# Performance work log

Hardware: AMD Instinct MI355X
Metric: run time of the kernel (lower is better)

Reference implementation:

```python
import jax, jax.numpy as jnp
import numpy as np

N = 100000      # nodes
E = 1600000     # edges (avg degree 16)
NX = 3          # input feature dim (data.x.shape[1])
K = 2           # number of kernels (len(kernel_DD) = manifold dim)
ORDER = 2       # par['order']
DEPTH = 2       # par['depth']
EPS = 1e-12     # F.normalize eps


def setup_inputs() -> dict:
    key = jax.random.key(0)
    ks = jax.random.split(key, 10)
    x = jax.random.normal(ks[0], (N, NX), dtype=jnp.float32)
    # per-edge kernel weights for the k directional kernels (sparse N x N ops)
    K_DD_vals = 0.1 * jax.random.normal(ks[1], (K, E), dtype=jnp.float32)
    K_DA_vals = 0.1 * jax.random.normal(ks[2], (K, E), dtype=jnp.float32)
    # lin[0]: in = 18*k = 36, out = 72
    lin0_w = 0.05 * jax.random.normal(ks[3], (36, 72), dtype=jnp.float32)
    lin0_b = jnp.zeros((72,), dtype=jnp.float32)
    # MLP: 144 -> 128 -> 64
    mlp_w1 = 0.05 * jax.random.normal(ks[4], (144, 128), dtype=jnp.float32)
    mlp_b1 = jnp.zeros((128,), dtype=jnp.float32)
    mlp_w2 = 0.05 * jax.random.normal(ks[5], (128, 64), dtype=jnp.float32)
    mlp_b2 = jnp.zeros((64,), dtype=jnp.float32)
    src = jax.random.randint(ks[6], (E,), 0, N, dtype=jnp.int32)
    dst = jnp.sort(jax.random.randint(ks[7], (E,), 0, N, dtype=jnp.int32))
    return {"x": x, "K_DD_vals": K_DD_vals, "K_DA_vals": K_DA_vals,
            "lin0_w": lin0_w, "lin0_b": lin0_b,
            "mlp_w1": mlp_w1, "mlp_b1": mlp_b1,
            "mlp_w2": mlp_w2, "mlp_b2": mlp_b2,
            "src": src, "dst": dst}


def _aniso_conv(h, src, dst, k_vals):
    """Kernel-weighted message passing: out_j[t] = sum_{e: dst[e]=t} K_j[e] * h[src[e]].
    Concatenate the k kernel outputs along the channel dim ([N, C] -> [N, k*C])."""
    msgs = h[src]  # [E, C] gather (shared across kernels)
    outs = [jax.ops.segment_sum(k_vals[j][:, None] * msgs, dst, num_segments=N)
            for j in range(k_vals.shape[0])]
    return jnp.concatenate(outs, axis=1)


def reference(x, K_DD_vals, K_DA_vals, lin0_w, lin0_b,
              mlp_w1, mlp_b1, mlp_w2, mlp_b2, src, dst):
    # --- DD phase (order hops), collecting per-hop outputs ---
    h = x
    collected = []
    for _ in range(ORDER):
        h = _aniso_conv(h, src, dst, K_DD_vals)   # channels *= K each hop
        collected.append(h)
    h = jnp.concatenate(collected, axis=1)        # [N, NX*(K + K^2)] = [N, 18]

    # --- DA phase (depth hops) with Linear+ReLU between hops ---
    for i in range(DEPTH):
        h = _aniso_conv(h, src, dst, K_DA_vals)
        if i < DEPTH - 1:
            h = jax.nn.relu(h @ lin0_w + lin0_b)  # 36 -> 72

    # --- MLP head: 144 -> 128 -> 64 ---
    h = jax.nn.relu(h @ mlp_w1 + mlp_b1)
    h = h @ mlp_w2 + mlp_b2

    # --- L2 normalize (F.normalize, p=2, dim=-1) ---
    norm = jnp.maximum(jnp.linalg.norm(h, axis=-1, keepdims=True), EPS)
    return h / norm
```

## Files before the change

kernel.cpp:

```cpp
#include <hip/hip_runtime.h>

#define N_NODES 100000
#define N_EDGES 1600000

typedef __attribute__((ext_vector_type(8))) short short8;
typedef __attribute__((ext_vector_type(4))) float f32x4;
typedef __attribute__((ext_vector_type(2))) unsigned short ushort2v;
typedef __attribute__((ext_vector_type(4))) unsigned short ushort4v;
typedef __attribute__((ext_vector_type(8))) unsigned short ushort8v;

static __device__ inline unsigned short f2bf(float f) {
    union { float f; unsigned u; } v; v.f = f;
    unsigned r = v.u + 0x7FFF + ((v.u >> 16) & 1);
    return (unsigned short)(r >> 16);
}
static __device__ inline float bf2f(unsigned short u) {
    union { unsigned u; float f; } v; v.u = ((unsigned)u) << 16;
    return v.f;
}

__global__ __launch_bounds__(256) void rowptr_k(const int* __restrict__ dst,
                                                int* __restrict__ rp) {
    int t = blockIdx.x * blockDim.x + threadIdx.x;
    if (t > N_NODES) return;
    int lo = 0, hi = N_EDGES;
    while (lo < hi) {
        int mid = (lo + hi) >> 1;
        if (dst[mid] < t) lo = mid + 1; else hi = mid;
    }
    rp[t] = lo;
}

__global__ __launch_bounds__(256) void prep_k(const float* __restrict__ w1,
                                              const float* __restrict__ w2,
                                              const float* __restrict__ l0w,
                                              unsigned short* __restrict__ w1t,
                                              unsigned short* __restrict__ w2t,
                                              unsigned short* __restrict__ w0t) {
    int id = blockIdx.x * blockDim.x + threadIdx.x;
    if (id < 128 * 160) {
        int o = id / 160, k = id - o * 160;
        w1t[id] = (k < 144) ? f2bf(w1[k * 128 + o]) : (unsigned short)0;
    } else if (id < 128 * 160 + 64 * 128) {
        int j = id - 128 * 160;
        int o = j / 128, k = j - o * 128;
        w2t[j] = f2bf(w2[k * 64 + o]);
    } else if (id < 128 * 160 + 64 * 128 + 80 * 64) {
        int j = id - 128 * 160 - 64 * 128;
        int o = j / 64, k = j - o * 64;
        w0t[j] = (o < 72 && k < 36) ? f2bf(l0w[k * 72 + o]) : (unsigned short)0;
    }
}

template<int VEC> struct VecU;
template<> struct VecU<1> { using T = unsigned short; };
template<> struct VecU<2> { using T = ushort2v; };
template<> struct VecU<4> { using T = ushort4v; };
template<> struct VecU<8> { using T = ushort8v; };

template<int OUT_STRIDE>
__global__ __launch_bounds__(256) void conv1_k(const float* __restrict__ hin,
                                               const float* __restrict__ kv,
                                               const int* __restrict__ src,
                                               const int* __restrict__ rp,
                                               unsigned short* __restrict__ hout) {
    int id = blockIdx.x * blockDim.x + threadIdx.x;
    if (id >= N_NODES * 3) return;
    int t = id / 3;
    int c = id - t * 3;
    int e0 = rp[t], e1 = rp[t + 1];
    float a0 = 0.f, a1 = 0.f;
    int e = e0;
    for (; e + 8 <= e1; e += 8) {
        int s[8]; float k0[8], k1[8], v[8];
#pragma unroll
        for (int u = 0; u < 8; ++u) s[u]  = src[e + u];
#pragma unroll
        for (int u = 0; u < 8; ++u) k0[u] = kv[e + u];
#pragma unroll
        for (int u = 0; u < 8; ++u) k1[u] = kv[N_EDGES + e + u];
#pragma unroll
        for (int u = 0; u < 8; ++u) v[u]  = hin[(size_t)s[u] * 3 + c];
#pragma unroll
        for (int u = 0; u < 8; ++u) { a0 += k0[u] * v[u]; a1 += k1[u] * v[u]; }
    }
    for (; e < e1; ++e) {
        int s = src[e];
        float v = hin[(size_t)s * 3 + c];
        a0 += kv[e] * v;
        a1 += kv[N_EDGES + e] * v;
    }
    hout[(size_t)t * OUT_STRIDE + c]     = f2bf(a0);
    hout[(size_t)t * OUT_STRIDE + 3 + c] = f2bf(a1);
}

template<int C, int VEC, int IN_STRIDE, int OUT_STRIDE, int OUT_OFF,
         int PAD_FROM, int PAD_TO>
__global__ __launch_bounds__(256) void convb_k(const unsigned short* __restrict__ hin,
                                               const float* __restrict__ kv,
                                               const int* __restrict__ src,
                                               const int* __restrict__ rp,
                                               unsigned short* __restrict__ hout) {
    constexpr int G = C / VEC;
    using VT = typename VecU<VEC>::T;
    int id = blockIdx.x * blockDim.x + threadIdx.x;
    if (id >= N_NODES * G) return;
    int t = id / G;
    int g = id - t * G;
    int c0 = g * VEC;
    int e0 = rp[t], e1 = rp[t + 1];

    float a0[VEC], a1[VEC];
#pragma unroll
    for (int q = 0; q < VEC; ++q) { a0[q] = 0.f; a1[q] = 0.f; }

    int e = e0;
    for (; e + 8 <= e1; e += 8) {
        int s[8]; float k0[8], k1[8];
#pragma unroll
        for (int u = 0; u < 8; ++u) s[u]  = src[e + u];
#pragma unroll
        for (int u = 0; u < 8; ++u) k0[u] = kv[e + u];
#pragma unroll
        for (int u = 0; u < 8; ++u) k1[u] = kv[N_EDGES + e + u];
        VT v[8];
#pragma unroll
        for (int u = 0; u < 8; ++u)
            v[u] = *reinterpret_cast<const VT*>(hin + (size_t)s[u] * IN_STRIDE + c0);
#pragma unroll
        for (int u = 0; u < 8; ++u) {
            const unsigned short* vf = reinterpret_cast<const unsigned short*>(&v[u]);
#pragma unroll
            for (int q = 0; q < VEC; ++q) {
                float x = bf2f(vf[q]);
                a0[q] += k0[u] * x;
                a1[q] += k1[u] * x;
            }
        }
    }
    for (; e < e1; ++e) {
        int s = src[e];
        float k0 = kv[e], k1 = kv[N_EDGES + e];
        VT v = *reinterpret_cast<const VT*>(hin + (size_t)s * IN_STRIDE + c0);
        const unsigned short* vf = reinterpret_cast<const unsigned short*>(&v);
#pragma unroll
        for (int q = 0; q < VEC; ++q) {
            float x = bf2f(vf[q]);
            a0[q] += k0 * x;
            a1[q] += k1 * x;
        }
    }

    VT r0, r1;
    unsigned short* r0f = reinterpret_cast<unsigned short*>(&r0);
    unsigned short* r1f = reinterpret_cast<unsigned short*>(&r1);
#pragma unroll
    for (int q = 0; q < VEC; ++q) { r0f[q] = f2bf(a0[q]); r1f[q] = f2bf(a1[q]); }
    *reinterpret_cast<VT*>(hout + (size_t)t * OUT_STRIDE + OUT_OFF + c0)     = r0;
    *reinterpret_cast<VT*>(hout + (size_t)t * OUT_STRIDE + OUT_OFF + C + c0) = r1;

    if constexpr (PAD_TO > PAD_FROM) {
        if (g == G - 1) {
            ushort4v z = {0, 0, 0, 0};
#pragma unroll
            for (int j = PAD_FROM; j < PAD_TO; j += 4)
                *reinterpret_cast<ushort4v*>(hout + (size_t)t * OUT_STRIDE + j) = z;
        }
    }
}

__global__ __launch_bounds__(256) void lin0m_k(const unsigned short* __restrict__ h3b,
                                               const unsigned short* __restrict__ w0t,
                                               const float* __restrict__ b0,
                                               unsigned short* __restrict__ h4b) {
    int tid = threadIdx.x;
    int w = tid >> 6;
    int lane = tid & 63;
    int lr = lane & 15;
    int kg = lane >> 4;
    int row_base = blockIdx.x * 64 + w * 16;

    f32x4 acc[5];
#pragma unroll
    for (int n = 0; n < 5; ++n) acc[n] = (f32x4){0.f, 0.f, 0.f, 0.f};

    const unsigned short* arow = h3b + (size_t)(row_base + lr) * 64 + kg * 8;
#pragma unroll
    for (int ks = 0; ks < 2; ++ks) {
        short8 a = *reinterpret_cast<const short8*>(arow + ks * 32);
#pragma unroll
        for (int n = 0; n < 5; ++n) {
            short8 b = *reinterpret_cast<const short8*>(w0t + (n * 16 + lr) * 64 + ks * 32 + kg * 8);
            acc[n] = __builtin_amdgcn_mfma_f32_16x16x32_bf16(a, b, acc[n], 0, 0, 0);
        }
    }
#pragma unroll
    for (int n = 0; n < 5; ++n) {
        int col = n * 16 + lr;
        if (col < 72) {
            float bv = b0[col];
#pragma unroll
            for (int q = 0; q < 4; ++q) {
                int t = row_base + kg * 4 + q;
                if (t < N_NODES)
                    h4b[(size_t)t * 72 + col] = f2bf(fmaxf(acc[n][q] + bv, 0.f));
            }
        }
    }
}

#define FH 168
#define HSTRIDE 136
__global__ __launch_bounds__(256) void fused_k(const unsigned short* __restrict__ h4b,
                                               const float* __restrict__ kv,
                                               const int* __restrict__ src,
                                               const int* __restrict__ rp,
                                               const unsigned short* __restrict__ w1t,
                                               const float* __restrict__ b1,
                                               const unsigned short* __restrict__ w2t,
                                               const float* __restrict__ b2,
                                               float* __restrict__ out) {
    __shared__ unsigned short sh[64 * FH];
    __shared__ unsigned short shid[64 * HSTRIDE];
    int tid = threadIdx.x;
    int node0 = blockIdx.x * 64;

    for (int task = tid; task < 576; task += 256) {
        int nd = task / 9;
        int g  = task - nd * 9;
        int t  = node0 + nd;
        int c0 = g * 8;
        int e0 = 0, e1 = 0;
        if (t < N_NODES) { e0 = rp[t]; e1 = rp[t + 1]; }

        float a0[8], a1[8];
#pragma unroll
        for (int q = 0; q < 8; ++q) { a0[q] = 0.f; a1[q] = 0.f; }

        int e = e0;
        for (; e + 8 <= e1; e += 8) {
            int s[8]; float k0[8], k1[8];
#pragma unroll
            for (int u = 0; u < 8; ++u) s[u]  = src[e + u];
#pragma unroll
            for (int u = 0; u < 8; ++u) k0[u] = kv[e + u];
#pragma unroll
            for (int u = 0; u < 8; ++u) k1[u] = kv[N_EDGES + e + u];
            ushort8v v[8];
#pragma unroll
            for (int u = 0; u < 8; ++u)
                v[u] = *reinterpret_cast<const ushort8v*>(h4b + (size_t)s[u] * 72 + c0);
#pragma unroll
            for (int u = 0; u < 8; ++u) {
#pragma unroll
                for (int q = 0; q < 8; ++q) {
                    float x = bf2f(v[u][q]);
                    a0[q] += k0[u] * x;
                    a1[q] += k1[u] * x;
                }
            }
        }
        for (; e < e1; ++e) {
            int s = src[e];
            float k0 = kv[e], k1 = kv[N_EDGES + e];
            ushort8v v = *reinterpret_cast<const ushort8v*>(h4b + (size_t)s * 72 + c0);
#pragma unroll
            for (int q = 0; q < 8; ++q) {
                float x = bf2f(v[q]);
                a0[q] += k0 * x;
                a1[q] += k1 * x;
            }
        }

        ushort8v r0, r1;
#pragma unroll
        for (int q = 0; q < 8; ++q) { r0[q] = f2bf(a0[q]); r1[q] = f2bf(a1[q]); }
        *reinterpret_cast<ushort8v*>(sh + nd * FH + c0)      = r0;
        *reinterpret_cast<ushort8v*>(sh + nd * FH + 72 + c0) = r1;
    }
    for (int i = tid; i < 128; i += 256) {
        int nd = i >> 1, half = i & 1;
        ushort8v z = {0, 0, 0, 0, 0, 0, 0, 0};
        *reinterpret_cast<ushort8v*>(sh + nd * FH + 144 + half * 8) = z;
    }
    __syncthreads();

    int w = tid >> 6;
    int lane = tid & 63;
    int lr = lane & 15;
    int kg = lane >> 4;
    int row_base = node0 + w * 16;

    f32x4 acc[8];
#pragma unroll
    for (int n = 0; n < 8; ++n) acc[n] = (f32x4){0.f, 0.f, 0.f, 0.f};

    const unsigned short* arow = sh + (w * 16 + lr) * FH + kg * 8;
#pragma unroll
    for (int ks = 0; ks < 5; ++ks) {
        short8 a = *reinterpret_cast<const short8*>(arow + ks * 32);
#pragma unroll
        for (int n = 0; n < 8; ++n) {
            short8 b = *reinterpret_cast<const short8*>(w1t + (n * 16 + lr) * 160 + ks * 32 + kg * 8);
            acc[n] = __builtin_amdgcn_mfma_f32_16x16x32_bf16(a, b, acc[n], 0, 0, 0);
        }
    }
#pragma unroll
    for (int n = 0; n < 8; ++n) {
        float bv = b1[n * 16 + lr];
#pragma unroll
        for (int q = 0; q < 4; ++q) {
            float hv = fmaxf(acc[n][q] + bv, 0.f);
            shid[(w * 16 + kg * 4 + q) * HSTRIDE + n * 16 + lr] = f2bf(hv);
        }
    }
    __syncthreads();

    f32x4 acc2[4];
#pragma unroll
    for (int n = 0; n < 4; ++n) acc2[n] = (f32x4){0.f, 0.f, 0.f, 0.f};
#pragma unroll
    for (int ks = 0; ks < 4; ++ks) {
        short8 a = *reinterpret_cast<const short8*>(shid + (w * 16 + lr) * HSTRIDE + ks * 32 + kg * 8);
#pragma unroll
        for (int n = 0; n < 4; ++n) {
            short8 b = *reinterpret_cast<const short8*>(w2t + (n * 16 + lr) * 128 + ks * 32 + kg * 8);
            acc2[n] = __builtin_amdgcn_mfma_f32_16x16x32_bf16(a, b, acc2[n], 0, 0, 0);
        }
    }

    float v[4][4];
    float ss[4];
#pragma unroll
    for (int q = 0; q < 4; ++q) ss[q] = 0.f;
#pragma unroll
    for (int n = 0; n < 4; ++n) {
        float bv = b2[n * 16 + lr];
#pragma unroll
        for (int q = 0; q < 4; ++q) {
            float x = acc2[n][q] + bv;
            v[n][q] = x;
            ss[q] += x * x;
        }
    }
#pragma unroll
    for (int q = 0; q < 4; ++q) {
#pragma unroll
        for (int d = 1; d < 16; d <<= 1) ss[q] += __shfl_xor(ss[q], d);
    }
#pragma unroll
    for (int q = 0; q < 4; ++q) {
        int node = row_base + kg * 4 + q;
        if (node < N_NODES) {
            float scale = 1.f / fmaxf(sqrtf(ss[q]), 1e-12f);
#pragma unroll
            for (int n = 0; n < 4; ++n)
                out[(size_t)node * 64 + n * 16 + lr] = v[n][q] * scale;
        }
    }
}

extern "C" void kernel_launch(void* const* d_in, const int* in_sizes, int n_in,
                              void* d_out, int out_size, void* d_ws, size_t ws_size,
                              hipStream_t stream) {
    const float* x   = (const float*)d_in[0];
    const float* kdd = (const float*)d_in[1];
    const float* kda = (const float*)d_in[2];
    const float* l0w = (const float*)d_in[3];
    const float* l0b = (const float*)d_in[4];
    const float* w1  = (const float*)d_in[5];
    const float* b1  = (const float*)d_in[6];
    const float* w2  = (const float*)d_in[7];
    const float* b2  = (const float*)d_in[8];
    const int*   src = (const int*)d_in[9];
    const int*   dst = (const int*)d_in[10];
    float* out = (float*)d_out;
    char* ws = (char*)d_ws;

    int*   rp  = (int*)ws;
    unsigned short* w0t = (unsigned short*)(ws + 400384u);
    unsigned short* w1t = (unsigned short*)(ws + 410624u);
    unsigned short* w2t = (unsigned short*)(ws + 451584u);
    unsigned short* hcb = (unsigned short*)(ws + 475136u);
    unsigned short* h3b = (unsigned short*)(ws + 4480000u);
    unsigned short* h4b = (unsigned short*)(ws + 17284096u);

    rowptr_k<<<(N_NODES + 1 + 255) / 256, 256, 0, stream>>>(dst, rp);
    prep_k<<<(128 * 160 + 64 * 128 + 80 * 64 + 255) / 256, 256, 0, stream>>>(w1, w2, l0w, w1t, w2t, w0t);

    conv1_k<20><<<(N_NODES * 3 + 255) / 256, 256, 0, stream>>>(x, kdd, src, rp, hcb);
    convb_k<6, 2, 20, 20, 6, 0, 0><<<(N_NODES * 3 + 255) / 256, 256, 0, stream>>>(hcb, kdd, src, rp, hcb);

    convb_k<18, 2, 20, 64, 0, 36, 64><<<(N_NODES * 9 + 255) / 256, 256, 0, stream>>>(hcb, kda, src, rp, h3b);
    lin0m_k<<<(N_NODES + 63) / 64, 256, 0, stream>>>(h3b, w0t, l0b, h4b);

    fused_k<<<(N_NODES + 63) / 64, 256, 0, stream>>>(h4b, kda, src, rp, w1t, b1, w2t, b2, out);
}
```

Before: 206.9 us.

## Use one thread per node for early convs and unfuse final conv from MLP

The first three message-passing hops now assign a single thread to each destination node and gather that node's whole bf16 feature row. Before, several threads per node each reloaded the same src indices and kernel weights. The input x is first packed into a padded 4-wide bf16 array so it can be read as one vector. The last aggregation hop is split out of the fused MLP kernel into a generic vectorised conv that writes a padded 160-wide intermediate, followed by a separate MFMA-based MLP kernel. This cuts redundant index and weight loads, but launches far fewer threads for the early hops, holds more registers per thread, and adds a global round trip for the final hop's output.

```diff
diff --git a/kernel.cpp b/kernel.cpp
--- a/kernel.cpp
+++ b/kernel.cpp
@@ -52,47 +52,233 @@
     }
 }
 
+__global__ __launch_bounds__(256) void x2b_k(const float* __restrict__ x,
+                                             unsigned short* __restrict__ xb4) {
+    int t = blockIdx.x * blockDim.x + threadIdx.x;
+    if (t >= N_NODES) return;
+    ushort4v w;
+    w[0] = f2bf(x[(size_t)t * 3 + 0]);
+    w[1] = f2bf(x[(size_t)t * 3 + 1]);
+    w[2] = f2bf(x[(size_t)t * 3 + 2]);
+    w[3] = 0;
+    *reinterpret_cast<ushort4v*>(xb4 + (size_t)t * 4) = w;
+}
+
+__global__ __launch_bounds__(256) void conv1n_k(const unsigned short* __restrict__ xb4,
+                                                const float* __restrict__ kv,
+                                                const int* __restrict__ src,
+                                                const int* __restrict__ rp,
+                                                unsigned short* __restrict__ hcb) {
+    int t = blockIdx.x * blockDim.x + threadIdx.x;
+    if (t >= N_NODES) return;
+    int e0 = rp[t], e1 = rp[t + 1];
+    float a0[3] = {0.f, 0.f, 0.f}, a1[3] = {0.f, 0.f, 0.f};
+    int e = e0;
+    for (; e + 8 <= e1; e += 8) {
+        int s[8]; float k0[8], k1[8];
+#pragma unroll
+        for (int u = 0; u < 8; ++u) s[u]  = src[e + u];
+#pragma unroll
+        for (int u = 0; u < 8; ++u) k0[u] = kv[e + u];
+#pragma unroll
+        for (int u = 0; u < 8; ++u) k1[u] = kv[N_EDGES + e + u];
+        ushort4v v[8];
+#pragma unroll
+        for (int u = 0; u < 8; ++u)
+            v[u] = *reinterpret_cast<const ushort4v*>(xb4 + (size_t)s[u] * 4);
+#pragma unroll
+        for (int u = 0; u < 8; ++u) {
+#pragma unroll
+            for (int q = 0; q < 3; ++q) {
+                float x = bf2f(v[u][q]);
+                a0[q] += k0[u] * x;
+                a1[q] += k1[u] * x;
+            }
+        }
+    }
+    for (; e < e1; ++e) {
+        int s = src[e];
+        float k0 = kv[e], k1 = kv[N_EDGES + e];
+        ushort4v v = *reinterpret_cast<const ushort4v*>(xb4 + (size_t)s * 4);
+#pragma unroll
+        for (int q = 0; q < 3; ++q) {
+            float x = bf2f(v[q]);
+            a0[q] += k0 * x;
+            a1[q] += k1 * x;
+        }
+    }
+    ushort4v r0; ushort2v r1;
+    r0[0] = f2bf(a0[0]); r0[1] = f2bf(a0[1]); r0[2] = f2bf(a0[2]); r0[3] = f2bf(a1[0]);
+    r1[0] = f2bf(a1[1]); r1[1] = f2bf(a1[2]);
+    *reinterpret_cast<ushort4v*>(hcb + (size_t)t * 20)     = r0;
+    *reinterpret_cast<ushort2v*>(hcb + (size_t)t * 20 + 4) = r1;
+}
+
+__global__ __launch_bounds__(256) void conv2n_k(const unsigned short* __restrict__ hcbr,
+                                                const float* __restrict__ kv,
+                                                const int* __restrict__ src,
+                                                const int* __restrict__ rp,
+                                                unsigned short* __restrict__ hcbw) {
+    int t = blockIdx.x * blockDim.x + threadIdx.x;
+    if (t >= N_NODES) return;
+    int e0 = rp[t], e1 = rp[t + 1];
+    float a0[6], a1[6];
+#pragma unroll
+    for (int q = 0; q < 6; ++q) { a0[q] = 0.f; a1[q] = 0.f; }
+    int e = e0;
+    for (; e + 8 <= e1; e += 8) {
+        int s[8]; float k0[8], k1[8];
+#pragma unroll
+        for (int u = 0; u < 8; ++u) s[u]  = src[e + u];
+#pragma unroll
+        for (int u = 0; u < 8; ++u) k0[u] = kv[e + u];
+#pragma unroll
+        for (int u = 0; u < 8; ++u) k1[u] = kv[N_EDGES + e + u];
+        ushort4v va[8]; ushort2v vb[8];
+#pragma unroll
+        for (int u = 0; u < 8; ++u) {
+            const unsigned short* b = hcbr + (size_t)s[u] * 20;
+            va[u] = *reinterpret_cast<const ushort4v*>(b);
+            vb[u] = *reinterpret_cast<const ushort2v*>(b + 4);
+        }
+#pragma unroll
+        for (int u = 0; u < 8; ++u) {
+#pragma unroll
+            for (int q = 0; q < 4; ++q) {
+                float x = bf2f(va[u][q]);
+                a0[q] += k0[u] * x;
+                a1[q] += k1[u] * x;
+            }
+#pragma unroll
+            for (int q = 0; q < 2; ++q) {
+                float x = bf2f(vb[u][q]);
+                a0[4 + q] += k0[u] * x;
+                a1[4 + q] += k1[u] * x;
+            }
+        }
+    }
+    for (; e < e1; ++e) {
+        int s = src[e];
+        float k0 = kv[e], k1 = kv[N_EDGES + e];
+        const unsigned short* b = hcbr + (size_t)s * 20;
+        ushort4v va = *reinterpret_cast<const ushort4v*>(b);
+        ushort2v vb = *reinterpret_cast<const ushort2v*>(b + 4);
+#pragma unroll
+        for (int q = 0; q < 4; ++q) {
+            float x = bf2f(va[q]);
+            a0[q] += k0 * x; a1[q] += k1 * x;
+        }
+#pragma unroll
+        for (int q = 0; q < 2; ++q) {
+            float x = bf2f(vb[q]);
+            a0[4 + q] += k0 * x; a1[4 + q] += k1 * x;
+        }
+    }
+    unsigned short* o = hcbw + (size_t)t * 20;
+#pragma unroll
+    for (int p = 0; p < 3; ++p) {
+        ushort2v w0; w0[0] = f2bf(a0[p * 2]); w0[1] = f2bf(a0[p * 2 + 1]);
+        *reinterpret_cast<ushort2v*>(o + 6 + p * 2) = w0;
+        ushort2v w1; w1[0] = f2bf(a1[p * 2]); w1[1] = f2bf(a1[p * 2 + 1]);
+        *reinterpret_cast<ushort2v*>(o + 12 + p * 2) = w1;
+    }
+}
+
+__global__ __launch_bounds__(256) void conv3n_k(const unsigned short* __restrict__ hcb,
+                                                const float* __restrict__ kv,
+                                                const int* __restrict__ src,
+                                                const int* __restrict__ rp,
+                                                unsigned short* __restrict__ h3b) {
+    int t = blockIdx.x * blockDim.x + threadIdx.x;
+    if (t >= N_NODES) return;
+    int e0 = rp[t], e1 = rp[t + 1];
+    float a0[18], a1[18];
+#pragma unroll
+    for (int q = 0; q < 18; ++q) { a0[q] = 0.f; a1[q] = 0.f; }
+    int e = e0;
+    for (; e + 4 <= e1; e += 4) {
+        int s[4]; float k0[4], k1[4];
+#pragma unroll
+        for (int u = 0; u < 4; ++u) s[u]  = src[e + u];
+#pragma unroll
+        for (int u = 0; u < 4; ++u) k0[u] = kv[e + u];
+#pragma unroll
+        for (int u = 0; u < 4; ++u) k1[u] = kv[N_EDGES + e + u];
+        ushort8v p0[4], p1[4]; ushort2v p2[4];
+#pragma unroll
+        for (int u = 0; u < 4; ++u) {
+            const unsigned short* b = hcb + (size_t)s[u] * 20;
+            p0[u] = *reinterpret_cast<const ushort8v*>(b);
+            p1[u] = *reinterpret_cast<const ushort8v*>(b + 8);
+            p2[u] = *reinterpret_cast<const ushort2v*>(b + 16);
+        }
+#pragma unroll
+        for (int u = 0; u < 4; ++u) {
+#pragma unroll
+            for (int q = 0; q < 8; ++q) {
+                float x = bf2f(p0[u][q]);
+                a0[q] += k0[u] * x; a1[q] += k1[u] * x;
+            }
+#pragma unroll
+            for (int q = 0; q < 8; ++q) {
+                float x = bf2f(p1[u][q]);
+                a0[8 + q] += k0[u] * x; a1[8 + q] += k1[u] * x;
+            }
+#pragma unroll
+            for (int q = 0; q < 2; ++q) {
+                float x = bf2f(p2[u][q]);
+                a0[16 + q] += k0[u] * x; a1[16 + q] += k1[u] * x;
+            }
+        }
+    }
+    for (; e < e1; ++e) {
+        int s = src[e];
+        float k0 = kv[e], k1 = kv[N_EDGES + e];
+        const unsigned short* b = hcb + (size_t)s * 20;
+        ushort8v p0 = *reinterpret_cast<const ushort8v*>(b);
+        ushort8v p1 = *reinterpret_cast<const ushort8v*>(b + 8);
+        ushort2v p2 = *reinterpret_cast<const ushort2v*>(b + 16);
+#pragma unroll
+        for (int q = 0; q < 8; ++q) {
+            float x = bf2f(p0[q]); a0[q] += k0 * x; a1[q] += k1 * x;
+        }
+#pragma unroll
+        for (int q = 0; q < 8; ++q) {
+            float x = bf2f(p1[q]); a0[8 + q] += k0 * x; a1[8 + q] += k1 * x;
+        }
+#pragma unroll
+        for (int q = 0; q < 2; ++q) {
+            float x = bf2f(p2[q]); a0[16 + q] += k0 * x; a1[16 + q] += k1 * x;
+        }
+    }
+    unsigned short* o = h3b + (size_t)t * 64;
+    unsigned short r[36];
+#pragma unroll
+    for (int q = 0; q < 18; ++q) r[q] = f2bf(a0[q]);
+#pragma unroll
+    for (int q = 0; q < 18; ++q) r[18 + q] = f2bf(a1[q]);
+#pragma unroll
+    for (int p = 0; p < 4; ++p) {
+        ushort8v w;
+#pragma unroll
+        for (int q = 0; q < 8; ++q) w[q] = r[p * 8 + q];
+        *reinterpret_cast<ushort8v*>(o + p * 8) = w;
+    }
+    {
+        ushort4v w;
+#pragma unroll
+        for (int q = 0; q < 4; ++q) w[q] = r[32 + q];
+        *reinterpret_cast<ushort4v*>(o + 32) = w;
+    }
+    ushort4v z = {0, 0, 0, 0};
+#pragma unroll
+    for (int j = 36; j < 64; j += 4)
+        *reinterpret_cast<ushort4v*>(o + j) = z;
+}
+
 template<int VEC> struct VecU;
-template<> struct VecU<1> { using T = unsigned short; };
-template<> struct VecU<2> { using T = ushort2v; };
 template<> struct VecU<4> { using T = ushort4v; };
 template<> struct VecU<8> { using T = ushort8v; };
-
-template<int OUT_STRIDE>
-__global__ __launch_bounds__(256) void conv1_k(const float* __restrict__ hin,
-                                               const float* __restrict__ kv,
-                                               const int* __restrict__ src,
-                                               const int* __restrict__ rp,
-                                               unsigned short* __restrict__ hout) {
-    int id = blockIdx.x * blockDim.x + threadIdx.x;
-    if (id >= N_NODES * 3) return;
-    int t = id / 3;
-    int c = id - t * 3;
-    int e0 = rp[t], e1 = rp[t + 1];
-    float a0 = 0.f, a1 = 0.f;
-    int e = e0;
-    for (; e + 8 <= e1; e += 8) {
-        int s[8]; float k0[8], k1[8], v[8];
-#pragma unroll
-        for (int u = 0; u < 8; ++u) s[u]  = src[e + u];
-#pragma unroll
-        for (int u = 0; u < 8; ++u) k0[u] = kv[e + u];
-#pragma unroll
-        for (int u = 0; u < 8; ++u) k1[u] = kv[N_EDGES + e + u];
-#pragma unroll
-        for (int u = 0; u < 8; ++u) v[u]  = hin[(size_t)s[u] * 3 + c];
-#pragma unroll
-        for (int u = 0; u < 8; ++u) { a0 += k0[u] * v[u]; a1 += k1[u] * v[u]; }
-    }
-    for (; e < e1; ++e) {
-        int s = src[e];
-        float v = hin[(size_t)s * 3 + c];
-        a0 += kv[e] * v;
-        a1 += kv[N_EDGES + e] * v;
-    }
-    hout[(size_t)t * OUT_STRIDE + c]     = f2bf(a0);
-    hout[(size_t)t * OUT_STRIDE + 3 + c] = f2bf(a1);
-}
 
 template<int C, int VEC, int IN_STRIDE, int OUT_STRIDE, int OUT_OFF,
          int PAD_FROM, int PAD_TO>
@@ -129,10 +315,9 @@
             v[u] = *reinterpret_cast<const VT*>(hin + (size_t)s[u] * IN_STRIDE + c0);
 #pragma unroll
         for (int u = 0; u < 8; ++u) {
-            const unsigned short* vf = reinterpret_cast<const unsigned short*>(&v[u]);
 #pragma unroll
             for (int q = 0; q < VEC; ++q) {
-                float x = bf2f(vf[q]);
+                float x = bf2f(v[u][q]);
                 a0[q] += k0[u] * x;
                 a1[q] += k1[u] * x;
             }
@@ -142,20 +327,17 @@
         int s = src[e];
         float k0 = kv[e], k1 = kv[N_EDGES + e];
         VT v = *reinterpret_cast<const VT*>(hin + (size_t)s * IN_STRIDE + c0);
-        const unsigned short* vf = reinterpret_cast<const unsigned short*>(&v);
 #pragma unroll
         for (int q = 0; q < VEC; ++q) {
-            float x = bf2f(vf[q]);
+            float x = bf2f(v[q]);
             a0[q] += k0 * x;
             a1[q] += k1 * x;
         }
     }
 
     VT r0, r1;
-    unsigned short* r0f = reinterpret_cast<unsigned short*>(&r0);
-    unsigned short* r1f = reinterpret_cast<unsigned short*>(&r1);
-#pragma unroll
-    for (int q = 0; q < VEC; ++q) { r0f[q] = f2bf(a0[q]); r1f[q] = f2bf(a1[q]); }
+#pragma unroll
+    for (int q = 0; q < VEC; ++q) { r0[q] = f2bf(a0[q]); r1[q] = f2bf(a1[q]); }
     *reinterpret_cast<VT*>(hout + (size_t)t * OUT_STRIDE + OUT_OFF + c0)     = r0;
     *reinterpret_cast<VT*>(hout + (size_t)t * OUT_STRIDE + OUT_OFF + C + c0) = r1;
 
@@ -209,93 +391,26 @@
     }
 }
 
-#define FH 168
 #define HSTRIDE 136
-__global__ __launch_bounds__(256) void fused_k(const unsigned short* __restrict__ h4b,
-                                               const float* __restrict__ kv,
-                                               const int* __restrict__ src,
-                                               const int* __restrict__ rp,
-                                               const unsigned short* __restrict__ w1t,
-                                               const float* __restrict__ b1,
-                                               const unsigned short* __restrict__ w2t,
-                                               const float* __restrict__ b2,
-                                               float* __restrict__ out) {
-    __shared__ unsigned short sh[64 * FH];
-    __shared__ unsigned short shid[64 * HSTRIDE];
+__global__ __launch_bounds__(256) void mlp_k(const unsigned short* __restrict__ h5b,
+                                             const unsigned short* __restrict__ w1t,
+                                             const float* __restrict__ b1,
+                                             const unsigned short* __restrict__ w2t,
+                                             const float* __restrict__ b2,
+                                             float* __restrict__ out) {
+    __shared__ unsigned short sh[64 * HSTRIDE];
     int tid = threadIdx.x;
-    int node0 = blockIdx.x * 64;
-
-    for (int task = tid; task < 576; task += 256) {
-        int nd = task / 9;
-        int g  = task - nd * 9;
-        int t  = node0 + nd;
-        int c0 = g * 8;
-        int e0 = 0, e1 = 0;
-        if (t < N_NODES) { e0 = rp[t]; e1 = rp[t + 1]; }
-
-        float a0[8], a1[8];
-#pragma unroll
-        for (int q = 0; q < 8; ++q) { a0[q] = 0.f; a1[q] = 0.f; }
-
-        int e = e0;
-        for (; e + 8 <= e1; e += 8) {
-            int s[8]; float k0[8], k1[8];
-#pragma unroll
-            for (int u = 0; u < 8; ++u) s[u]  = src[e + u];
-#pragma unroll
-            for (int u = 0; u < 8; ++u) k0[u] = kv[e + u];
-#pragma unroll
-            for (int u = 0; u < 8; ++u) k1[u] = kv[N_EDGES + e + u];
-            ushort8v v[8];
-#pragma unroll
-            for (int u = 0; u < 8; ++u)
-                v[u] = *reinterpret_cast<const ushort8v*>(h4b + (size_t)s[u] * 72 + c0);
-#pragma unroll
-            for (int u = 0; u < 8; ++u) {
-#pragma unroll
-                for (int q = 0; q < 8; ++q) {
-                    float x = bf2f(v[u][q]);
-                    a0[q] += k0[u] * x;
-                    a1[q] += k1[u] * x;
-                }
-            }
-        }
-        for (; e < e1; ++e) {
-            int s = src[e];
-            float k0 = kv[e], k1 = kv[N_EDGES + e];
-            ushort8v v = *reinterpret_cast<const ushort8v*>(h4b + (size_t)s * 72 + c0);
-#pragma unroll
-            for (int q = 0; q < 8; ++q) {
-                float x = bf2f(v[q]);
-                a0[q] += k0 * x;
-                a1[q] += k1 * x;
-            }
-        }
-
-        ushort8v r0, r1;
-#pragma unroll
-        for (int q = 0; q < 8; ++q) { r0[q] = f2bf(a0[q]); r1[q] = f2bf(a1[q]); }
-        *reinterpret_cast<ushort8v*>(sh + nd * FH + c0)      = r0;
-        *reinterpret_cast<ushort8v*>(sh + nd * FH + 72 + c0) = r1;
-    }
-    for (int i = tid; i < 128; i += 256) {
-        int nd = i >> 1, half = i & 1;
-        ushort8v z = {0, 0, 0, 0, 0, 0, 0, 0};
-        *reinterpret_cast<ushort8v*>(sh + nd * FH + 144 + half * 8) = z;
-    }
-    __syncthreads();
-
     int w = tid >> 6;
     int lane = tid & 63;
     int lr = lane & 15;
     int kg = lane >> 4;
-    int row_base = node0 + w * 16;
+    int row_base = blockIdx.x * 64 + w * 16;
 
     f32x4 acc[8];
 #pragma unroll
     for (int n = 0; n < 8; ++n) acc[n] = (f32x4){0.f, 0.f, 0.f, 0.f};
 
-    const unsigned short* arow = sh + (w * 16 + lr) * FH + kg * 8;
+    const unsigned short* arow = h5b + (size_t)(row_base + lr) * 160 + kg * 8;
 #pragma unroll
     for (int ks = 0; ks < 5; ++ks) {
         short8 a = *reinterpret_cast<const short8*>(arow + ks * 32);
@@ -311,7 +426,7 @@
 #pragma unroll
         for (int q = 0; q < 4; ++q) {
             float hv = fmaxf(acc[n][q] + bv, 0.f);
-            shid[(w * 16 + kg * 4 + q) * HSTRIDE + n * 16 + lr] = f2bf(hv);
+            sh[(w * 16 + kg * 4 + q) * HSTRIDE + n * 16 + lr] = f2bf(hv);
         }
     }
     __syncthreads();
@@ -321,7 +436,7 @@
     for (int n = 0; n < 4; ++n) acc2[n] = (f32x4){0.f, 0.f, 0.f, 0.f};
 #pragma unroll
     for (int ks = 0; ks < 4; ++ks) {
-        short8 a = *reinterpret_cast<const short8*>(shid + (w * 16 + lr) * HSTRIDE + ks * 32 + kg * 8);
+        short8 a = *reinterpret_cast<const short8*>(sh + (w * 16 + lr) * HSTRIDE + ks * 32 + kg * 8);
 #pragma unroll
         for (int n = 0; n < 4; ++n) {
             short8 b = *reinterpret_cast<const short8*>(w2t + (n * 16 + lr) * 128 + ks * 32 + kg * 8);
@@ -384,15 +499,20 @@
     unsigned short* hcb = (unsigned short*)(ws + 475136u);
     unsigned short* h3b = (unsigned short*)(ws + 4480000u);
     unsigned short* h4b = (unsigned short*)(ws + 17284096u);
-
+    unsigned short* h5b = (unsigned short*)(ws + 31684096u);
+    unsigned short* xb4 = (unsigned short*)(ws + 31684096u);
+
+    int nb = (N_NODES + 255) / 256;
     rowptr_k<<<(N_NODES + 1 + 255) / 256, 256, 0, stream>>>(dst, rp);
     prep_k<<<(128 * 160 + 64 * 128 + 80 * 64 + 255) / 256, 256, 0, stream>>>(w1, w2, l0w, w1t, w2t, w0t);
-
-    conv1_k<20><<<(N_NODES * 3 + 255) / 256, 256, 0, stream>>>(x, kdd, src, rp, hcb);
-    convb_k<6, 2, 20, 20, 6, 0, 0><<<(N_NODES * 3 + 255) / 256, 256, 0, stream>>>(hcb, kdd, src, rp, hcb);
-
-    convb_k<18, 2, 20, 64, 0, 36, 64><<<(N_NODES * 9 + 255) / 256, 256, 0, stream>>>(hcb, kda, src, rp, h3b);
+    x2b_k<<<nb, 256, 0, stream>>>(x, xb4);
+
+    conv1n_k<<<nb, 256, 0, stream>>>(xb4, kdd, src, rp, hcb);
+    conv2n_k<<<nb, 256, 0, stream>>>(hcb, kdd, src, rp, hcb);
+
+    conv3n_k<<<nb, 256, 0, stream>>>(hcb, kda, src, rp, h3b);
     lin0m_k<<<(N_NODES + 63) / 64, 256, 0, stream>>>(h3b, w0t, l0b, h4b);
-
-    fused_k<<<(N_NODES + 63) / 64, 256, 0, stream>>>(h4b, kda, src, rp, w1t, b1, w2t, b2, out);
-}
+    convb_k<72, 8, 72, 160, 0, 144, 160><<<(N_NODES * 9 + 255) / 256, 256, 0, stream>>>(h4b, kda, src, rp, h5b);
+
+    mlp_k<<<(N_NODES + 63) / 64, 256, 0, stream>>>(h5b, w1t, b1, w2t, b2, out);
+}
```

After: 216.5 us. 1.05x slower.

## Fuse DD hop-2 with first DA hop on hop-1 channels; split final conv from MLP

Applied to the files above, without the earlier changes.

Hop 2 of the DD phase and the part of DA hop 1 that reads the hop-1 channels now run in one kernel. Each gathered hop-1 value feeds both kernel weight pairs, so those columns are gathered once instead of twice. The rest of DA hop 1 (hop-2 channels) gets its own kernel. The last DA conv moves out of the fused MLP kernel into a standalone grid-wide convb kernel that writes h5b to global memory, and the MLP kernel reads that buffer. This buys more parallelism for the final gather but adds an extra global round trip of a [N,160] bf16 buffer plus one more launch.

```diff
diff --git a/kernel.cpp b/kernel.cpp
--- a/kernel.cpp
+++ b/kernel.cpp
@@ -52,18 +52,11 @@
     }
 }
 
-template<int VEC> struct VecU;
-template<> struct VecU<1> { using T = unsigned short; };
-template<> struct VecU<2> { using T = ushort2v; };
-template<> struct VecU<4> { using T = ushort4v; };
-template<> struct VecU<8> { using T = ushort8v; };
-
-template<int OUT_STRIDE>
-__global__ __launch_bounds__(256) void conv1_k(const float* __restrict__ hin,
+__global__ __launch_bounds__(256) void conv1_k(const float* __restrict__ x,
                                                const float* __restrict__ kv,
                                                const int* __restrict__ src,
                                                const int* __restrict__ rp,
-                                               unsigned short* __restrict__ hout) {
+                                               unsigned short* __restrict__ hcb) {
     int id = blockIdx.x * blockDim.x + threadIdx.x;
     if (id >= N_NODES * 3) return;
     int t = id / 3;
@@ -80,19 +73,146 @@
 #pragma unroll
         for (int u = 0; u < 8; ++u) k1[u] = kv[N_EDGES + e + u];
 #pragma unroll
-        for (int u = 0; u < 8; ++u) v[u]  = hin[(size_t)s[u] * 3 + c];
+        for (int u = 0; u < 8; ++u) v[u]  = x[(size_t)s[u] * 3 + c];
 #pragma unroll
         for (int u = 0; u < 8; ++u) { a0 += k0[u] * v[u]; a1 += k1[u] * v[u]; }
     }
     for (; e < e1; ++e) {
         int s = src[e];
-        float v = hin[(size_t)s * 3 + c];
+        float v = x[(size_t)s * 3 + c];
         a0 += kv[e] * v;
         a1 += kv[N_EDGES + e] * v;
     }
-    hout[(size_t)t * OUT_STRIDE + c]     = f2bf(a0);
-    hout[(size_t)t * OUT_STRIDE + 3 + c] = f2bf(a1);
-}
+    hcb[(size_t)t * 20 + c]     = f2bf(a0);
+    hcb[(size_t)t * 20 + 3 + c] = f2bf(a1);
+}
+
+__global__ __launch_bounds__(256) void f23a_k(const unsigned short* __restrict__ hcbr,
+                                              const float* __restrict__ kdd,
+                                              const float* __restrict__ kda,
+                                              const int* __restrict__ src,
+                                              const int* __restrict__ rp,
+                                              unsigned short* __restrict__ hcbw,
+                                              unsigned short* __restrict__ h3b) {
+    int id = blockIdx.x * blockDim.x + threadIdx.x;
+    if (id >= N_NODES * 3) return;
+    int t = id / 3;
+    int g = id - t * 3;
+    int c0 = g * 2;
+    int e0 = rp[t], e1 = rp[t + 1];
+
+    float dd0[2] = {0.f, 0.f}, dd1[2] = {0.f, 0.f};
+    float da0[2] = {0.f, 0.f}, da1[2] = {0.f, 0.f};
+
+    int e = e0;
+    for (; e + 8 <= e1; e += 8) {
+        int s[8]; float d0[8], d1[8], a0w[8], a1w[8];
+#pragma unroll
+        for (int u = 0; u < 8; ++u) s[u]   = src[e + u];
+#pragma unroll
+        for (int u = 0; u < 8; ++u) d0[u]  = kdd[e + u];
+#pragma unroll
+        for (int u = 0; u < 8; ++u) d1[u]  = kdd[N_EDGES + e + u];
+#pragma unroll
+        for (int u = 0; u < 8; ++u) a0w[u] = kda[e + u];
+#pragma unroll
+        for (int u = 0; u < 8; ++u) a1w[u] = kda[N_EDGES + e + u];
+        ushort2v v[8];
+#pragma unroll
+        for (int u = 0; u < 8; ++u)
+            v[u] = *reinterpret_cast<const ushort2v*>(hcbr + (size_t)s[u] * 20 + c0);
+#pragma unroll
+        for (int u = 0; u < 8; ++u) {
+            float x0 = bf2f(v[u][0]), x1 = bf2f(v[u][1]);
+            dd0[0] += d0[u] * x0;  dd0[1] += d0[u] * x1;
+            dd1[0] += d1[u] * x0;  dd1[1] += d1[u] * x1;
+            da0[0] += a0w[u] * x0; da0[1] += a0w[u] * x1;
+            da1[0] += a1w[u] * x0; da1[1] += a1w[u] * x1;
+        }
+    }
+    for (; e < e1; ++e) {
+        int s = src[e];
+        float d0 = kdd[e], d1 = kdd[N_EDGES + e];
+        float a0w = kda[e], a1w = kda[N_EDGES + e];
+        ushort2v v = *reinterpret_cast<const ushort2v*>(hcbr + (size_t)s * 20 + c0);
+        float x0 = bf2f(v[0]), x1 = bf2f(v[1]);
+        dd0[0] += d0 * x0;  dd0[1] += d0 * x1;
+        dd1[0] += d1 * x0;  dd1[1] += d1 * x1;
+        da0[0] += a0w * x0; da0[1] += a0w * x1;
+        da1[0] += a1w * x0; da1[1] += a1w * x1;
+    }
+
+    ushort2v w;
+    w[0] = f2bf(dd0[0]); w[1] = f2bf(dd0[1]);
+    *reinterpret_cast<ushort2v*>(hcbw + (size_t)t * 20 + 6 + c0) = w;
+    w[0] = f2bf(dd1[0]); w[1] = f2bf(dd1[1]);
+    *reinterpret_cast<ushort2v*>(hcbw + (size_t)t * 20 + 12 + c0) = w;
+    w[0] = f2bf(da0[0]); w[1] = f2bf(da0[1]);
+    *reinterpret_cast<ushort2v*>(h3b + (size_t)t * 64 + c0) = w;
+    w[0] = f2bf(da1[0]); w[1] = f2bf(da1[1]);
+    *reinterpret_cast<ushort2v*>(h3b + (size_t)t * 64 + 18 + c0) = w;
+}
+
+__global__ __launch_bounds__(256) void conv3b_k(const unsigned short* __restrict__ hcb,
+                                                const float* __restrict__ kda,
+                                                const int* __restrict__ src,
+                                                const int* __restrict__ rp,
+                                                unsigned short* __restrict__ h3b) {
+    int id = blockIdx.x * blockDim.x + threadIdx.x;
+    if (id >= N_NODES * 6) return;
+    int t = id / 6;
+    int g = id - t * 6;
+    int c0 = g * 2;
+    int e0 = rp[t], e1 = rp[t + 1];
+
+    float da0[2] = {0.f, 0.f}, da1[2] = {0.f, 0.f};
+
+    int e = e0;
+    for (; e + 8 <= e1; e += 8) {
+        int s[8]; float a0w[8], a1w[8];
+#pragma unroll
+        for (int u = 0; u < 8; ++u) s[u]   = src[e + u];
+#pragma unroll
+        for (int u = 0; u < 8; ++u) a0w[u] = kda[e + u];
+#pragma unroll
+        for (int u = 0; u < 8; ++u) a1w[u] = kda[N_EDGES + e + u];
+        ushort2v v[8];
+#pragma unroll
+        for (int u = 0; u < 8; ++u)
+            v[u] = *reinterpret_cast<const ushort2v*>(hcb + (size_t)s[u] * 20 + 6 + c0);
+#pragma unroll
+        for (int u = 0; u < 8; ++u) {
+            float x0 = bf2f(v[u][0]), x1 = bf2f(v[u][1]);
+            da0[0] += a0w[u] * x0; da0[1] += a0w[u] * x1;
+            da1[0] += a1w[u] * x0; da1[1] += a1w[u] * x1;
+        }
+    }
+    for (; e < e1; ++e) {
+        int s = src[e];
+        float a0w = kda[e], a1w = kda[N_EDGES + e];
+        ushort2v v = *reinterpret_cast<const ushort2v*>(hcb + (size_t)s * 20 + 6 + c0);
+        float x0 = bf2f(v[0]), x1 = bf2f(v[1]);
+        da0[0] += a0w * x0; da0[1] += a0w * x1;
+        da1[0] += a1w * x0; da1[1] += a1w * x1;
+    }
+
+    ushort2v w;
+    w[0] = f2bf(da0[0]); w[1] = f2bf(da0[1]);
+    *reinterpret_cast<ushort2v*>(h3b + (size_t)t * 64 + 6 + c0) = w;
+    w[0] = f2bf(da1[0]); w[1] = f2bf(da1[1]);
+    *reinterpret_cast<ushort2v*>(h3b + (size_t)t * 64 + 24 + c0) = w;
+
+    if (g == 5) {
+        ushort4v z = {0, 0, 0, 0};
+#pragma unroll
+        for (int j = 36; j < 64; j += 4)
+            *reinterpret_cast<ushort4v*>(h3b + (size_t)t * 64 + j) = z;
+    }
+}
+
+template<int VEC> struct VecU;
+template<> struct VecU<4> { using T = ushort4v; };
+template<> struct VecU<8> { using T = ushort8v; };
 
 template<int C, int VEC, int IN_STRIDE, int OUT_STRIDE, int OUT_OFF,
          int PAD_FROM, int PAD_TO>
@@ -129,10 +249,9 @@
             v[u] = *reinterpret_cast<const VT*>(hin + (size_t)s[u] * IN_STRIDE + c0);
 #pragma unroll
         for (int u = 0; u < 8; ++u) {
-            const unsigned short* vf = reinterpret_cast<const unsigned short*>(&v[u]);
 #pragma unroll
             for (int q = 0; q < VEC; ++q) {
-                float x = bf2f(vf[q]);
+                float x = bf2f(v[u][q]);
                 a0[q] += k0[u] * x;
                 a1[q] += k1[u] * x;
             }
@@ -142,20 +261,17 @@
         int s = src[e];
         float k0 = kv[e], k1 = kv[N_EDGES + e];
         VT v = *reinterpret_cast<const VT*>(hin + (size_t)s * IN_STRIDE + c0);
-        const unsigned short* vf = reinterpret_cast<const unsigned short*>(&v);
 #pragma unroll
         for (int q = 0; q < VEC; ++q) {
-            float x = bf2f(vf[q]);
+            float x = bf2f(v[q]);
             a0[q] += k0 * x;
             a1[q] += k1 * x;
         }
     }
 
     VT r0, r1;
-    unsigned short* r0f = reinterpret_cast<unsigned short*>(&r0);
-    unsigned short* r1f = reinterpret_cast<unsigned short*>(&r1);
-#pragma unroll
-    for (int q = 0; q < VEC; ++q) { r0f[q] = f2bf(a0[q]); r1f[q] = f2bf(a1[q]); }
+#pragma unroll
+    for (int q = 0; q < VEC; ++q) { r0[q] = f2bf(a0[q]); r1[q] = f2bf(a1[q]); }
     *reinterpret_cast<VT*>(hout + (size_t)t * OUT_STRIDE + OUT_OFF + c0)     = r0;
     *reinterpret_cast<VT*>(hout + (size_t)t * OUT_STRIDE + OUT_OFF + C + c0) = r1;
 
@@ -209,93 +325,26 @@
     }
 }
 
-#define FH 168
 #define HSTRIDE 136
-__global__ __launch_bounds__(256) void fused_k(const unsigned short* __restrict__ h4b,
-                                               const float* __restrict__ kv,
-                                               const int* __restrict__ src,
-                                               const int* __restrict__ rp,
-                                               const unsigned short* __restrict__ w1t,
-                                               const float* __restrict__ b1,
-                                               const unsigned short* __restrict__ w2t,
-                                               const float* __restrict__ b2,
-                                               float* __restrict__ out) {
-    __shared__ unsigned short sh[64 * FH];
-    __shared__ unsigned short shid[64 * HSTRIDE];
+__global__ __launch_bounds__(256) void mlp_k(const unsigned short* __restrict__ h5b,
+                                             const unsigned short* __restrict__ w1t,
+                                             const float* __restrict__ b1,
+                                             const unsigned short* __restrict__ w2t,
+                                             const float* __restrict__ b2,
+                                             float* __restrict__ out) {
+    __shared__ unsigned short sh[64 * HSTRIDE];
     int tid = threadIdx.x;
-    int node0 = blockIdx.x * 64;
-
-    for (int task = tid; task < 576; task += 256) {
-        int nd = task / 9;
-        int g  = task - nd * 9;
-        int t  = node0 + nd;
-        int c0 = g * 8;
-        int e0 = 0, e1 = 0;
-        if (t < N_NODES) { e0 = rp[t]; e1 = rp[t + 1]; }
-
-        float a0[8], a1[8];
-#pragma unroll
-        for (int q = 0; q < 8; ++q) { a0[q] = 0.f; a1[q] = 0.f; }
-
-        int e = e0;
-        for (; e + 8 <= e1; e += 8) {
-            int s[8]; float k0[8], k1[8];
-#pragma unroll
-            for (int u = 0; u < 8; ++u) s[u]  = src[e + u];
-#pragma unroll
-            for (int u = 0; u < 8; ++u) k0[u] = kv[e + u];
-#pragma unroll
-            for (int u = 0; u < 8; ++u) k1[u] = kv[N_EDGES + e + u];
-            ushort8v v[8];
-#pragma unroll
-            for (int u = 0; u < 8; ++u)
-                v[u] = *reinterpret_cast<const ushort8v*>(h4b + (size_t)s[u] * 72 + c0);
-#pragma unroll
-            for (int u = 0; u < 8; ++u) {
-#pragma unroll
-                for (int q = 0; q < 8; ++q) {
-                    float x = bf2f(v[u][q]);
-                    a0[q] += k0[u] * x;
-                    a1[q] += k1[u] * x;
-                }
-            }
-        }
-        for (; e < e1; ++e) {
-            int s = src[e];
-            float k0 = kv[e], k1 = kv[N_EDGES + e];
-            ushort8v v = *reinterpret_cast<const ushort8v*>(h4b + (size_t)s * 72 + c0);
-#pragma unroll
-            for (int q = 0; q < 8; ++q) {
-                float x = bf2f(v[q]);
-                a0[q] += k0 * x;
-                a1[q] += k1 * x;
-            }
-        }
-
-        ushort8v r0, r1;
-#pragma unroll
-        for (int q = 0; q < 8; ++q) { r0[q] = f2bf(a0[q]); r1[q] = f2bf(a1[q]); }
-        *reinterpret_cast<ushort8v*>(sh + nd * FH + c0)      = r0;
-        *reinterpret_cast<ushort8v*>(sh + nd * FH + 72 + c0) = r1;
-    }
-    for (int i = tid; i < 128; i += 256) {
-        int nd = i >> 1, half = i & 1;
-        ushort8v z = {0, 0, 0, 0, 0, 0, 0, 0};
-        *reinterpret_cast<ushort8v*>(sh + nd * FH + 144 + half * 8) = z;
-    }
-    __syncthreads();
-
     int w = tid >> 6;
     int lane = tid & 63;
     int lr = lane & 15;
     int kg = lane >> 4;
-    int row_base = node0 + w * 16;
+    int row_base = blockIdx.x * 64 + w * 16;
 
     f32x4 acc[8];
 #pragma unroll
     for (int n = 0; n < 8; ++n) acc[n] = (f32x4){0.f, 0.f, 0.f, 0.f};
 
-    const unsigned short* arow = sh + (w * 16 + lr) * FH + kg * 8;
+    const unsigned short* arow = h5b + (size_t)(row_base + lr) * 160 + kg * 8;
 #pragma unroll
     for (int ks = 0; ks < 5; ++ks) {
         short8 a = *reinterpret_cast<const short8*>(arow + ks * 32);
@@ -311,7 +360,7 @@
 #pragma unroll
         for (int q = 0; q < 4; ++q) {
             float hv = fmaxf(acc[n][q] + bv, 0.f);
-            shid[(w * 16 + kg * 4 + q) * HSTRIDE + n * 16 + lr] = f2bf(hv);
+            sh[(w * 16 + kg * 4 + q) * HSTRIDE + n * 16 + lr] = f2bf(hv);
         }
     }
     __syncthreads();
@@ -321,7 +370,7 @@
     for (int n = 0; n < 4; ++n) acc2[n] = (f32x4){0.f, 0.f, 0.f, 0.f};
 #pragma unroll
     for (int ks = 0; ks < 4; ++ks) {
-        short8 a = *reinterpret_cast<const short8*>(shid + (w * 16 + lr) * HSTRIDE + ks * 32 + kg * 8);
+        short8 a = *reinterpret_cast<const short8*>(sh + (w * 16 + lr) * HSTRIDE + ks * 32 + kg * 8);
 #pragma unroll
         for (int n = 0; n < 4; ++n) {
             short8 b = *reinterpret_cast<const short8*>(w2t + (n * 16 + lr) * 128 + ks * 32 + kg * 8);
@@ -384,15 +433,17 @@
     unsigned short* hcb = (unsigned short*)(ws + 475136u);
     unsigned short* h3b = (unsigned short*)(ws + 4480000u);
     unsigned short* h4b = (unsigned short*)(ws + 17284096u);
+    unsigned short* h5b = (unsigned short*)(ws + 31684096u);
 
     rowptr_k<<<(N_NODES + 1 + 255) / 256, 256, 0, stream>>>(dst, rp);
     prep_k<<<(128 * 160 + 64 * 128 + 80 * 64 + 255) / 256, 256, 0, stream>>>(w1, w2, l0w, w1t, w2t, w0t);
 
-    conv1_k<20><<<(N_NODES * 3 + 255) / 256, 256, 0, stream>>>(x, kdd, src, rp, hcb);
-    convb_k<6, 2, 20, 20, 6, 0, 0><<<(N_NODES * 3 + 255) / 256, 256, 0, stream>>>(hcb, kdd, src, rp, hcb);
-
-    convb_k<18, 2, 20, 64, 0, 36, 64><<<(N_NODES * 9 + 255) / 256, 256, 0, stream>>>(hcb, kda, src, rp, h3b);
+    conv1_k<<<(N_NODES * 3 + 255) / 256, 256, 0, stream>>>(x, kdd, src, rp, hcb);
+    f23a_k<<<(N_NODES * 3 + 255) / 256, 256, 0, stream>>>(hcb, kdd, kda, src, rp, hcb, h3b);
+    conv3b_k<<<(N_NODES * 6 + 255) / 256, 256, 0, stream>>>(hcb, kda, src, rp, h3b);
+
     lin0m_k<<<(N_NODES + 63) / 64, 256, 0, stream>>>(h3b, w0t, l0b, h4b);
-
-    fused_k<<<(N_NODES + 63) / 64, 256, 0, stream>>>(h4b, kda, src, rp, w1t, b1, w2t, b2, out);
-}
+    convb_k<72, 8, 72, 160, 0, 144, 160><<<(N_NODES * 9 + 255) / 256, 256, 0, stream>>>(h4b, kda, src, rp, h5b);
+
+    mlp_k<<<(N_NODES + 63) / 64, 256, 0, stream>>>(h5b, w1t, b1, w2t, b2, out);
+}
```

New measurement: 207.4 us. Within noise of the previous version (+0.2%).
